# Optimization experiments

Hardware: AMD Instinct MI355X
Metric: run time of the kernel (lower is better)

The kernel has to match this reference:

```python
import jax, jax.numpy as jnp
import numpy as np

VOCAB = 50000
EMB = 200        # embedding_size
CAP = 3          # capitalization_size
IN = EMB + CAP   # LSTM input size = 203
HID = 128        # LSTMCell(128)
B = 256
T = 500          # comment_length
NC = 6           # num_classes
DENSE = 64


def _lstm_scan(x_tbi, W, b):
    """x_tbi: [T,B,IN]. W: [IN+HID, 4*HID] (tf gate order i, j, f, o), b: [4*HID].
    Returns h sequence [T,B,HID]. forget_bias=1.0 as in tf.contrib.rnn.LSTMCell."""
    h0 = jnp.zeros((x_tbi.shape[1], HID), x_tbi.dtype)

    def step(carry, x):
        h, c = carry
        gates = jnp.concatenate([x, h], axis=-1) @ W + b   # [B, 4*HID]
        i, j, f, o = jnp.split(gates, 4, axis=-1)
        c = jax.nn.sigmoid(f + 1.0) * c + jax.nn.sigmoid(i) * jnp.tanh(j)
        h = jax.nn.sigmoid(o) * jnp.tanh(c)
        return (h, c), h

    _, hs = jax.lax.scan(step, (h0, h0), x_tbi)
    return hs


def setup_inputs() -> dict:
    key = jax.random.key(0)
    ks = jax.random.split(key, 12)
    words = jax.random.randint(ks[0], (B, T), 0, VOCAB, dtype=jnp.int32)
    capitals = jax.random.randint(ks[1], (B, T), 0, CAP, dtype=jnp.int32)
    # word embeddings: random trainable table with a trailing zero-padding row
    word_emb = jax.random.normal(ks[2], (VOCAB + 1, EMB), dtype=jnp.float32) * 0.1
    # capitalization embedding: one_hot_embedding_matrix(3) = [eye(3); zeros(1,3)]
    cap_emb = jnp.concatenate([jnp.eye(CAP, dtype=jnp.float32),
                               jnp.zeros((1, CAP), dtype=jnp.float32)], axis=0)
    def glorot(k, shape):
        lim = np.sqrt(6.0 / (shape[0] + shape[1]))
        return jax.random.uniform(k, shape, jnp.float32, -lim, lim)
    W_fw = glorot(ks[3], (IN + HID, 4 * HID))
    b_fw = jnp.zeros((4 * HID,), jnp.float32)
    W_bw = glorot(ks[4], (IN + HID, 4 * HID))
    b_bw = jnp.zeros((4 * HID,), jnp.float32)
    W1 = glorot(ks[5], (2 * HID, DENSE))
    b1 = jnp.zeros((DENSE,), jnp.float32)
    W2 = glorot(ks[6], (DENSE, NC))
    b2 = jnp.zeros((NC,), jnp.float32)
    return {"words": words, "capitals": capitals, "word_emb": word_emb,
            "cap_emb": cap_emb, "W_fw": W_fw, "b_fw": b_fw,
            "W_bw": W_bw, "b_bw": b_bw, "W1": W1, "b1": b1,
            "W2": W2, "b2": b2}


def reference(words, capitals, word_emb, cap_emb, W_fw, b_fw, W_bw, b_bw,
              W1, b1, W2, b2):
    # embedding lookups and concat -> [B, T, 203]
    x = jnp.concatenate([word_emb[words], cap_emb[capitals]], axis=-1)
    x_tbi = jnp.transpose(x, (1, 0, 2))                    # [T, B, IN]
    # forward direction: take output at last timestep
    h_fw_last = _lstm_scan(x_tbi, W_fw, b_fw)[-1]          # [B, HID]
    # backward direction: bidirectional_dynamic_rnn reverses bw outputs back,
    # so outputs[1][:, 0, :] == last state of scan over the reversed sequence
    h_bw_first = _lstm_scan(x_tbi[::-1], W_bw, b_bw)[-1]   # [B, HID]
    rnn_output = jnp.concatenate([h_fw_last, h_bw_first], axis=1)  # [B, 256]
    dense1 = jax.nn.elu(rnn_output @ W1 + b1)              # [B, 64]
    y_hat = jax.nn.sigmoid(dense1 @ W2 + b2)               # [B, NC]
    return y_hat
```

## Files before the change

### kernel.cpp

```cpp
#include <hip/hip_runtime.h>

#define T 500
#define NB 256
#define VROWS 50001
#define EMB 200
#define KPAD 224
#define LOG2E 1.44269504f

typedef unsigned short u16;
typedef __attribute__((ext_vector_type(8))) __bf16 bf16x8;
typedef __attribute__((ext_vector_type(8))) short short8;
typedef __attribute__((ext_vector_type(8))) u16 u16x8;
typedef __attribute__((ext_vector_type(4))) float f32x4;
typedef __attribute__((ext_vector_type(4))) u16 u16x4;

#define AS1 __attribute__((address_space(1)))
#define AS3 __attribute__((address_space(3)))

__device__ __forceinline__ u16 f2bf(float x) {
  __bf16 h = (__bf16)x;
  return __builtin_bit_cast(u16, h);
}
__device__ __forceinline__ float bf2f(u16 b) {
  union { unsigned u; float f; } v; v.u = ((unsigned)b) << 16;
  return v.f;
}
__device__ __forceinline__ float rcp_(float x) { return __builtin_amdgcn_rcpf(x); }
__device__ __forceinline__ float ex2_(float x) { return __builtin_amdgcn_exp2f(x); }
__device__ __forceinline__ float gsc(int g) { return (g == 1) ? 2.f * LOG2E : -LOG2E; }

__global__ void prep_kernel(const float* __restrict__ cap_emb,
                            const float* __restrict__ Wfw, const float* __restrict__ bfw,
                            const float* __restrict__ Wbw, const float* __restrict__ bbw,
                            float* __restrict__ Cproj, u16* __restrict__ Bt) {
  const int S2 = 2 * 512 * KPAD;
  const int S3 = 2 * 4 * 512;
  int tid = blockIdx.x * blockDim.x + threadIdx.x;
  int nthr = gridDim.x * blockDim.x;
  for (int i = tid; i < S2 + S3; i += nthr) {
    if (i < S2) {
      int d = i / (512 * KPAD), rem = i - d * (512 * KPAD);
      int colp = rem / KPAD, k = rem - colp * KPAD;
      const float* W = d ? Wbw : Wfw;
      int g = colp & 3, jj = colp >> 2;
      Bt[i] = (k < EMB) ? f2bf(W[k * 512 + g * 128 + jj] * gsc(g)) : (u16)0;
    } else {
      int idx = i - S2;
      int dir = idx >> 11; int c = (idx >> 9) & 3; int colp = idx & 511;
      int j = colp >> 2, g = colp & 3;
      const float* W = dir ? Wbw : Wfw;
      const float* bias = dir ? bbw : bfw;
      float v = bias[g * 128 + j] + (g == 2 ? 1.f : 0.f);
      #pragma unroll
      for (int cc = 0; cc < 3; ++cc)
        v += cap_emb[c * 3 + cc] * W[(200 + cc) * 512 + g * 128 + j];
      Cproj[idx] = v * gsc(g);
    }
  }
}

__global__ __launch_bounds__(256) void xproj_kernel(
    const int* __restrict__ words, const int* __restrict__ caps,
    const float* __restrict__ word_emb, const u16* __restrict__ Bt,
    const float* __restrict__ Cproj, u16* __restrict__ XP) {
  const int bid = blockIdx.x;
  const int xcd = bid & 7, slot = bid >> 3;
  const int mt = (slot >> 3) * 8 + xcd;
  const int inner = slot & 7;
  const int nt = inner & 3, dir = inner >> 2;

  const u16* __restrict__ B = Bt + (size_t)dir * 512 * KPAD;
  u16* __restrict__ xp = XP + (size_t)dir * T * NB * 512;

  __shared__ __align__(16) char pool[34048];
  u16* As = (u16*)pool;
  u16* Bs = (u16*)(pool + 16384);
  float (*Cls)[132] = (float(*)[132])pool;

  const int tid = threadIdx.x;
  const int w = tid >> 6, l = tid & 63;
  const int la = l & 15, lb = l >> 4;
  const int wr = w >> 1, wc = w & 1;
  const int tblk = mt >> 1;
  const int bbase = (mt & 1) * 128;
  const int n0 = nt * 128;

  const int arow = tid >> 1, khalf = tid & 1;
  const int wd = words[(bbase + arow) * T + tblk];
  const float* __restrict__ aemb = word_emb + (size_t)wd * EMB;
  const int aswz0 = (arow * 4 + ((khalf * 2 + 0) ^ (arow & 3))) * 8;
  const int aswz1 = (arow * 4 + ((khalf * 2 + 1) ^ (arow & 3))) * 8;

  const int s0 = w * 128 + l, s1 = w * 128 + 64 + l;
  const int brn0 = s0 >> 2, bc0 = (s0 & 3) ^ (brn0 & 3);
  const int brn1 = s1 >> 2, bc1 = (s1 & 3) ^ (brn1 & 3);
  const u16* bsrc0 = B + (size_t)(n0 + brn0) * KPAD + bc0 * 8;
  const u16* bsrc1 = B + (size_t)(n0 + brn1) * KPAD + bc1 * 8;

  f32x4 va[4];
  auto loadA = [&](int ks) {
    #pragma unroll
    for (int q = 0; q < 4; ++q)
      va[q] = *(const f32x4*)(aemb + ks * 32 + khalf * 16 + q * 4);
  };
  auto writeA = [&](int buf) {
    u16x8 lo, hi;
    #pragma unroll
    for (int e = 0; e < 4; ++e) {
      lo[e] = f2bf(va[0][e]); lo[4 + e] = f2bf(va[1][e]);
      hi[e] = f2bf(va[2][e]); hi[4 + e] = f2bf(va[3][e]);
    }
    *(u16x8*)&As[buf * 4096 + aswz0] = lo;
    *(u16x8*)&As[buf * 4096 + aswz1] = hi;
  };
  auto stageB = [&](int buf, int ks) {
    __builtin_amdgcn_global_load_lds(
        (const AS1 void*)(bsrc0 + ks * 32),
        (AS3 void*)&Bs[buf * 4096 + (w * 128) * 8], 16, 0, 0);
    __builtin_amdgcn_global_load_lds(
        (const AS1 void*)(bsrc1 + ks * 32),
        (AS3 void*)&Bs[buf * 4096 + (w * 128 + 64) * 8], 16, 0, 0);
  };

  f32x4 z = {0.f, 0.f, 0.f, 0.f};
  f32x4 acc[4][4] = {{z,z,z,z},{z,z,z,z},{z,z,z,z},{z,z,z,z}};

  loadA(0);
  stageB(0, 0);
  writeA(0);
  __syncthreads();

  #pragma unroll 1
  for (int ks = 0; ks < 7; ++ks) {
    const int cur = ks & 1;
    if (ks < 6) { stageB(cur ^ 1, ks + 1); loadA(ks + 1); }
    bf16x8 af[4], bfr[4];
    #pragma unroll
    for (int m = 0; m < 4; ++m) {
      int ra = wr * 64 + m * 16 + la;
      af[m] = *(const bf16x8*)&As[cur * 4096 + ra * 32 + ((lb ^ (ra & 3)) * 8)];
    }
    #pragma unroll
    for (int n = 0; n < 4; ++n) {
      int rn = wc * 64 + n * 16 + la;
      bfr[n] = *(const bf16x8*)&Bs[cur * 4096 + rn * 32 + ((lb ^ (rn & 3)) * 8)];
    }
    #pragma unroll
    for (int m = 0; m < 4; ++m)
      #pragma unroll
      for (int n = 0; n < 4; ++n)
        acc[m][n] = __builtin_amdgcn_mfma_f32_16x16x32_bf16(af[m], bfr[n], acc[m][n], 0, 0, 0);
    if (ks < 6) writeA(cur ^ 1);
    __syncthreads();
  }

  const int rrow = tid >> 1, rch = tid & 1;
  const int rb = bbase + rrow;
  const int rcap = caps[rb * T + tblk];
  const float* __restrict__ cbase = Cproj + (dir * 4 + rcap) * 512;
  u16* __restrict__ rop = xp + ((size_t)tblk * NB + rb) * 512;

  #pragma unroll
  for (int pass = 0; pass < 2; ++pass) {
    if (wc == pass) {
      #pragma unroll
      for (int m = 0; m < 4; ++m)
        #pragma unroll
        for (int n = 0; n < 4; ++n)
          *(f32x4*)&Cls[n * 16 + la][wr * 64 + m * 16 + lb * 4] = acc[m][n];
    }
    __syncthreads();
    int colp0 = n0 + pass * 64 + rch * 32;
    #pragma unroll
    for (int s = 0; s < 4; ++s) {
      u16x8 o;
      #pragma unroll
      for (int e = 0; e < 8; ++e) {
        int cl = rch * 32 + s * 8 + e;
        o[e] = f2bf(Cls[cl][rrow] + cbase[colp0 + s * 8 + e]);
      }
      *(u16x8*)(rop + colp0 + s * 8) = o;
    }
    __syncthreads();
  }
}

template <int PAR>
__device__ __forceinline__ void lstm_step(
    int t, int dir, int la, int lb, int j,
    const u16* __restrict__ xpd, int voff0, int voff1, int voff2, int voff3,
    const bf16x8 (&bfrag)[4][4], u16* __restrict__ hbuf,
    u16x4 (&xc)[4],
    u16x4 (&xg)[4],
    f32x4& cst, f32x4& hl) {
  const u16* hb = hbuf + PAR * 2048;
  const int swz = (la & 7) << 3;
  bf16x8 afr[4];
  #pragma unroll
  for (int kk = 0; kk < 4; ++kk)
    afr[kk] = *(const bf16x8*)(hb + ((la * 128 + kk * 32 + lb * 8) ^ swz));

  {
    int ts = t + 2; if (ts > T - 1) ts = T - 1;
    int tt = dir ? (T - 1 - ts) : ts;
    const u16* p = xpd + (size_t)tt * (NB * 512);
    xg[0] = *(const u16x4*)(p + voff0);
    xg[1] = *(const u16x4*)(p + voff1);
    xg[2] = *(const u16x4*)(p + voff2);
    xg[3] = *(const u16x4*)(p + voff3);
  }

  f32x4 acc0, acc1, acc2, acc3;
  #pragma unroll
  for (int r = 0; r < 4; ++r) {
    acc0[r] = bf2f(xc[r][0]);
    acc1[r] = bf2f(xc[r][1]);
    acc2[r] = bf2f(xc[r][2]);
    acc3[r] = bf2f(xc[r][3]);
  }
  __builtin_amdgcn_s_setprio(1);
  #pragma unroll
  for (int kk = 0; kk < 4; ++kk) {
    acc0 = __builtin_amdgcn_mfma_f32_16x16x32_bf16(afr[kk], bfrag[0][kk], acc0, 0, 0, 0);
    acc1 = __builtin_amdgcn_mfma_f32_16x16x32_bf16(afr[kk], bfrag[1][kk], acc1, 0, 0, 0);
    acc2 = __builtin_amdgcn_mfma_f32_16x16x32_bf16(afr[kk], bfrag[2][kk], acc2, 0, 0, 0);
    acc3 = __builtin_amdgcn_mfma_f32_16x16x32_bf16(afr[kk], bfrag[3][kk], acc3, 0, 0, 0);
  }
  __builtin_amdgcn_s_setprio(0);
  u16* ho = hbuf + (PAR ^ 1) * 2048;
  #pragma unroll
  for (int r = 0; r < 4; ++r) {
    float ei = ex2_(acc0[r]);
    float ej = ex2_(acc1[r]);
    float ef = ex2_(acc2[r]);
    float eo = ex2_(acc3[r]);
    float pij = (1.f + ei) * (1.f + ej);
    float pf  = 1.f + ef;
    float num = cst[r] * pij + (ej - 1.f) * pf;
    float cn  = num * rcp_(pij * pf);
    cst[r] = cn;
    float E = ex2_(2.f * LOG2E * cn);
    float hn = (E - 1.f) * rcp_((1.f + eo) * (1.f + E));
    hl[r] = hn;
    int row = lb * 4 + r;
    ho[(row * 128 + j) ^ ((row & 7) << 3)] = f2bf(hn);
  }
  __builtin_amdgcn_sched_barrier(0);
  asm volatile("s_waitcnt lgkmcnt(0)");
  __builtin_amdgcn_s_barrier();
  __builtin_amdgcn_sched_barrier(0);
}

__global__ __launch_bounds__(512, 1) void lstm_kernel(
    const u16* __restrict__ XP, const float* __restrict__ Wfw,
    const float* __restrict__ Wbw, float* __restrict__ rnn) {
  const int dir = blockIdx.x & 1;
  const int chunk = blockIdx.x >> 1;
  const int b0 = chunk * 16;
  const u16* __restrict__ xpd = XP + (size_t)dir * T * NB * 512;
  const float* __restrict__ W = dir ? Wbw : Wfw;

  const int tid = threadIdx.x;
  const int w = tid >> 6, l = tid & 63, la = l & 15, lb = l >> 4;
  const int j = w * 16 + la;

  const int voff0 = (b0 + lb * 4 + 0) * 512 + j * 4;
  const int voff1 = (b0 + lb * 4 + 1) * 512 + j * 4;
  const int voff2 = (b0 + lb * 4 + 2) * 512 + j * 4;
  const int voff3 = (b0 + lb * 4 + 3) * 512 + j * 4;

  bf16x8 bfrag[4][4];
  #pragma unroll
  for (int g = 0; g < 4; ++g) {
    #pragma unroll
    for (int kk = 0; kk < 4; ++kk) {
      short8 t8;
      #pragma unroll
      for (int r = 0; r < 8; ++r) {
        int k = kk * 32 + lb * 8 + r;
        t8[r] = (short)f2bf(W[(203 + k) * 512 + g * 128 + j] * gsc(g));
      }
      bfrag[g][kk] = __builtin_bit_cast(bf16x8, t8);
    }
  }

  __shared__ u16 hbuf[2 * 16 * 128];
  for (int i = tid; i < 2 * 16 * 128; i += 512) hbuf[i] = 0;

  f32x4 cst = {0.f, 0.f, 0.f, 0.f};
  f32x4 hl  = {0.f, 0.f, 0.f, 0.f};

  u16x4 xA[4], xB[4], xC[4], xD[4];
  {
    int tt0 = dir ? (T - 1) : 0;
    int tt1 = dir ? (T - 2) : 1;
    const u16* p0 = xpd + (size_t)tt0 * (NB * 512);
    const u16* p1 = xpd + (size_t)tt1 * (NB * 512);
    xA[0] = *(const u16x4*)(p0 + voff0); xA[1] = *(const u16x4*)(p0 + voff1);
    xA[2] = *(const u16x4*)(p0 + voff2); xA[3] = *(const u16x4*)(p0 + voff3);
    xB[0] = *(const u16x4*)(p1 + voff0); xB[1] = *(const u16x4*)(p1 + voff1);
    xB[2] = *(const u16x4*)(p1 + voff2); xB[3] = *(const u16x4*)(p1 + voff3);
  }
  __syncthreads();

  #pragma unroll 1
  for (int tq = 0; tq < T / 4; ++tq) {
    int t0 = 4 * tq;
    lstm_step<0>(t0,     dir, la, lb, j, xpd, voff0, voff1, voff2, voff3,
                 bfrag, hbuf, xA, xC, cst, hl);
    lstm_step<1>(t0 + 1, dir, la, lb, j, xpd, voff0, voff1, voff2, voff3,
                 bfrag, hbuf, xB, xD, cst, hl);
    lstm_step<0>(t0 + 2, dir, la, lb, j, xpd, voff0, voff1, voff2, voff3,
                 bfrag, hbuf, xC, xA, cst, hl);
    lstm_step<1>(t0 + 3, dir, la, lb, j, xpd, voff0, voff1, voff2, voff3,
                 bfrag, hbuf, xD, xB, cst, hl);
  }

  #pragma unroll
  for (int r = 0; r < 4; ++r)
    rnn[(size_t)(b0 + lb * 4 + r) * 256 + dir * 128 + j] = hl[r];
}

__global__ void head_kernel(const float* __restrict__ rnn, const float* __restrict__ W1,
                            const float* __restrict__ b1, const float* __restrict__ W2,
                            const float* __restrict__ b2, float* __restrict__ out) {
  int b = blockIdx.x;
  int jj = threadIdx.x;
  __shared__ float d1[64];
  float acc = b1[jj];
  const float* r = rnn + b * 256;
  #pragma unroll 4
  for (int k = 0; k < 256; ++k) acc += r[k] * W1[k * 64 + jj];
  d1[jj] = acc > 0.f ? acc : (__expf(acc) - 1.f);
  __syncthreads();
  if (jj < 6) {
    float a2 = b2[jj];
    #pragma unroll 8
    for (int k = 0; k < 64; ++k) a2 += d1[k] * W2[k * 6 + jj];
    out[b * 6 + jj] = rcp_(1.f + __expf(-a2));
  }
}

extern "C" void kernel_launch(void* const* d_in, const int* in_sizes, int n_in,
                              void* d_out, int out_size, void* d_ws, size_t ws_size,
                              hipStream_t stream) {
  (void)in_sizes; (void)n_in; (void)out_size; (void)ws_size;
  const int*   words    = (const int*)  d_in[0];
  const int*   caps     = (const int*)  d_in[1];
  const float* word_emb = (const float*)d_in[2];
  const float* cap_emb  = (const float*)d_in[3];
  const float* Wfw      = (const float*)d_in[4];
  const float* bfw      = (const float*)d_in[5];
  const float* Wbw      = (const float*)d_in[6];
  const float* bbw      = (const float*)d_in[7];
  const float* W1       = (const float*)d_in[8];
  const float* b1       = (const float*)d_in[9];
  const float* W2       = (const float*)d_in[10];
  const float* b2       = (const float*)d_in[11];
  float* out = (float*)d_out;

  char* base = (char*)d_ws;
  size_t off = 0;
  auto alloc = [&](size_t bytes) {
    char* q = base + off;
    off = (off + bytes + 255) & ~(size_t)255;
    return q;
  };
  u16*   XP     = (u16*)  alloc((size_t)2 * T * NB * 512 * 2);
  u16*   Bt     = (u16*)  alloc((size_t)2 * 512 * KPAD * 2);
  float* Cproj  = (float*)alloc((size_t)2 * 4 * 512 * 4);
  float* rnn    = (float*)alloc((size_t)256 * 256 * 4);

  hipLaunchKernelGGL(prep_kernel, dim3(256), dim3(256), 0, stream,
                     cap_emb, Wfw, bfw, Wbw, bbw, Cproj, Bt);
  hipLaunchKernelGGL(xproj_kernel, dim3(8000), dim3(256), 0, stream,
                     words, caps, word_emb, Bt, Cproj, XP);
  hipLaunchKernelGGL(lstm_kernel, dim3(32), dim3(512), 0, stream,
                     XP, Wfw, Wbw, rnn);
  hipLaunchKernelGGL(head_kernel, dim3(256), dim3(64), 0, stream,
                     rnn, W1, b1, W2, b2, out);
}
```

Baseline: 627.3 us.

## Stage embedding rows once per block and loop over all output tiles; transpose LSTM MFMA

The input-projection kernel now gathers the 128 embedding rows for a timestep block into shared memory once. It then loops over all eight direction/column tiles, instead of launching a separate block per tile that re-gathers the same rows. This removes redundant gather and bf16-conversion traffic, at the cost of fewer, larger 512-thread blocks and a big A buffer in LDS. The LSTM step swaps the MFMA operand order so each lane owns contiguous gate values for one batch row. That gives vectorized 16-byte XP loads, packed h stores to LDS and a vector store of the final state.

```diff
diff --git a/kernel.cpp b/kernel.cpp
--- a/kernel.cpp
+++ b/kernel.cpp
@@ -59,139 +59,126 @@
   }
 }
 
-__global__ __launch_bounds__(256) void xproj_kernel(
+__global__ __launch_bounds__(512) void xproj_kernel(
     const int* __restrict__ words, const int* __restrict__ caps,
     const float* __restrict__ word_emb, const u16* __restrict__ Bt,
     const float* __restrict__ Cproj, u16* __restrict__ XP) {
-  const int bid = blockIdx.x;
-  const int xcd = bid & 7, slot = bid >> 3;
-  const int mt = (slot >> 3) * 8 + xcd;
-  const int inner = slot & 7;
-  const int nt = inner & 3, dir = inner >> 2;
-
-  const u16* __restrict__ B = Bt + (size_t)dir * 512 * KPAD;
-  u16* __restrict__ xp = XP + (size_t)dir * T * NB * 512;
-
+  const int mt = blockIdx.x;
+  const int tblk = mt >> 1;
+  const int bbase = (mt & 1) * 128;
+
+  __shared__ __align__(16) u16 As[128 * 256];
   __shared__ __align__(16) char pool[34048];
-  u16* As = (u16*)pool;
-  u16* Bs = (u16*)(pool + 16384);
+  u16* Bs = (u16*)pool;
   float (*Cls)[132] = (float(*)[132])pool;
 
   const int tid = threadIdx.x;
   const int w = tid >> 6, l = tid & 63;
   const int la = l & 15, lb = l >> 4;
   const int wr = w >> 1, wc = w & 1;
-  const int tblk = mt >> 1;
-  const int bbase = (mt & 1) * 128;
-  const int n0 = nt * 128;
-
-  const int arow = tid >> 1, khalf = tid & 1;
-  const int wd = words[(bbase + arow) * T + tblk];
-  const float* __restrict__ aemb = word_emb + (size_t)wd * EMB;
-  const int aswz0 = (arow * 4 + ((khalf * 2 + 0) ^ (arow & 3))) * 8;
-  const int aswz1 = (arow * 4 + ((khalf * 2 + 1) ^ (arow & 3))) * 8;
-
-  const int s0 = w * 128 + l, s1 = w * 128 + 64 + l;
-  const int brn0 = s0 >> 2, bc0 = (s0 & 3) ^ (brn0 & 3);
-  const int brn1 = s1 >> 2, bc1 = (s1 & 3) ^ (brn1 & 3);
-  const u16* bsrc0 = B + (size_t)(n0 + brn0) * KPAD + bc0 * 8;
-  const u16* bsrc1 = B + (size_t)(n0 + brn1) * KPAD + bc1 * 8;
-
-  f32x4 va[4];
-  auto loadA = [&](int ks) {
-    #pragma unroll
-    for (int q = 0; q < 4; ++q)
-      va[q] = *(const f32x4*)(aemb + ks * 32 + khalf * 16 + q * 4);
-  };
-  auto writeA = [&](int buf) {
-    u16x8 lo, hi;
-    #pragma unroll
-    for (int e = 0; e < 4; ++e) {
-      lo[e] = f2bf(va[0][e]); lo[4 + e] = f2bf(va[1][e]);
-      hi[e] = f2bf(va[2][e]); hi[4 + e] = f2bf(va[3][e]);
-    }
-    *(u16x8*)&As[buf * 4096 + aswz0] = lo;
-    *(u16x8*)&As[buf * 4096 + aswz1] = hi;
-  };
-  auto stageB = [&](int buf, int ks) {
-    __builtin_amdgcn_global_load_lds(
-        (const AS1 void*)(bsrc0 + ks * 32),
-        (AS3 void*)&Bs[buf * 4096 + (w * 128) * 8], 16, 0, 0);
-    __builtin_amdgcn_global_load_lds(
-        (const AS1 void*)(bsrc1 + ks * 32),
-        (AS3 void*)&Bs[buf * 4096 + (w * 128 + 64) * 8], 16, 0, 0);
-  };
-
-  f32x4 z = {0.f, 0.f, 0.f, 0.f};
-  f32x4 acc[4][4] = {{z,z,z,z},{z,z,z,z},{z,z,z,z},{z,z,z,z}};
-
-  loadA(0);
-  stageB(0, 0);
-  writeA(0);
+
+  for (int i = tid; i < 128 * 28; i += 512) {
+    int r = i / 28, c = i - r * 28;
+    u16x8 o;
+    if (c < 25) {
+      int wd = words[(bbase + r) * T + tblk];
+      const float* p = word_emb + (size_t)wd * EMB + c * 8;
+      f32x4 v0 = *(const f32x4*)p;
+      f32x4 v1 = *(const f32x4*)(p + 4);
+      #pragma unroll
+      for (int e = 0; e < 4; ++e) { o[e] = f2bf(v0[e]); o[4 + e] = f2bf(v1[e]); }
+    } else {
+      o = u16x8{0,0,0,0,0,0,0,0};
+    }
+    *(u16x8*)&As[r * 256 + ((c ^ (r & 7)) * 8)] = o;
+  }
   __syncthreads();
 
-  #pragma unroll 1
-  for (int ks = 0; ks < 7; ++ks) {
-    const int cur = ks & 1;
-    if (ks < 6) { stageB(cur ^ 1, ks + 1); loadA(ks + 1); }
-    bf16x8 af[4], bfr[4];
-    #pragma unroll
-    for (int m = 0; m < 4; ++m) {
-      int ra = wr * 64 + m * 16 + la;
-      af[m] = *(const bf16x8*)&As[cur * 4096 + ra * 32 + ((lb ^ (ra & 3)) * 8)];
-    }
-    #pragma unroll
-    for (int n = 0; n < 4; ++n) {
-      int rn = wc * 64 + n * 16 + la;
-      bfr[n] = *(const bf16x8*)&Bs[cur * 4096 + rn * 32 + ((lb ^ (rn & 3)) * 8)];
-    }
-    #pragma unroll
-    for (int m = 0; m < 4; ++m)
-      #pragma unroll
-      for (int n = 0; n < 4; ++n)
-        acc[m][n] = __builtin_amdgcn_mfma_f32_16x16x32_bf16(af[m], bfr[n], acc[m][n], 0, 0, 0);
-    if (ks < 6) writeA(cur ^ 1);
-    __syncthreads();
-  }
-
-  const int rrow = tid >> 1, rch = tid & 1;
+  const int s_ = w * 64 + l;
+  const int brn = s_ >> 2, bd = s_ & 3;
+  const int bc = bd ^ (brn & 3);
+
+  const int rrow = tid >> 2, rch = tid & 3;
   const int rb = bbase + rrow;
   const int rcap = caps[rb * T + tblk];
-  const float* __restrict__ cbase = Cproj + (dir * 4 + rcap) * 512;
-  u16* __restrict__ rop = xp + ((size_t)tblk * NB + rb) * 512;
-
-  #pragma unroll
-  for (int pass = 0; pass < 2; ++pass) {
-    if (wc == pass) {
-      #pragma unroll
-      for (int m = 0; m < 4; ++m)
+
+  #pragma unroll 1
+  for (int combo = 0; combo < 8; ++combo) {
+    const int dir = combo >> 2, nt = combo & 3;
+    const u16* __restrict__ B = Bt + (size_t)dir * 512 * KPAD;
+    u16* __restrict__ xp = XP + (size_t)dir * T * NB * 512;
+    const int n0 = nt * 128;
+    const u16* bsrc = B + (size_t)(n0 + brn) * KPAD + bc * 8;
+
+    auto stageB = [&](int buf, int ks) {
+      __builtin_amdgcn_global_load_lds(
+          (const AS1 void*)(bsrc + ks * 32),
+          (AS3 void*)&Bs[buf * 4096 + w * 512], 16, 0, 0);
+    };
+
+    f32x4 z = {0.f, 0.f, 0.f, 0.f};
+    f32x4 acc[2][4] = {{z,z,z,z},{z,z,z,z}};
+
+    stageB(0, 0);
+    __syncthreads();
+    #pragma unroll 1
+    for (int ks = 0; ks < 7; ++ks) {
+      const int cur = ks & 1;
+      if (ks < 6) stageB(cur ^ 1, ks + 1);
+      bf16x8 af[2], bfr[4];
+      #pragma unroll
+      for (int m = 0; m < 2; ++m) {
+        int ra = wr * 32 + m * 16 + la;
+        af[m] = *(const bf16x8*)&As[ra * 256 + (((ks * 4 + lb) ^ (ra & 7)) * 8)];
+      }
+      #pragma unroll
+      for (int n = 0; n < 4; ++n) {
+        int rn = wc * 64 + n * 16 + la;
+        bfr[n] = *(const bf16x8*)&Bs[cur * 4096 + rn * 32 + ((lb ^ (rn & 3)) * 8)];
+      }
+      #pragma unroll
+      for (int m = 0; m < 2; ++m)
         #pragma unroll
         for (int n = 0; n < 4; ++n)
-          *(f32x4*)&Cls[n * 16 + la][wr * 64 + m * 16 + lb * 4] = acc[m][n];
-    }
-    __syncthreads();
-    int colp0 = n0 + pass * 64 + rch * 32;
+          acc[m][n] = __builtin_amdgcn_mfma_f32_16x16x32_bf16(af[m], bfr[n], acc[m][n], 0, 0, 0);
+      __syncthreads();
+    }
+
+    const float* __restrict__ cbase = Cproj + (dir * 4 + rcap) * 512;
+    u16* __restrict__ rop = xp + ((size_t)tblk * NB + rb) * 512;
     #pragma unroll
-    for (int s = 0; s < 4; ++s) {
-      u16x8 o;
-      #pragma unroll
-      for (int e = 0; e < 8; ++e) {
-        int cl = rch * 32 + s * 8 + e;
-        o[e] = f2bf(Cls[cl][rrow] + cbase[colp0 + s * 8 + e]);
-      }
-      *(u16x8*)(rop + colp0 + s * 8) = o;
-    }
-    __syncthreads();
+    for (int pass = 0; pass < 2; ++pass) {
+      if (wc == pass) {
+        #pragma unroll
+        for (int m = 0; m < 2; ++m)
+          #pragma unroll
+          for (int n = 0; n < 4; ++n)
+            *(f32x4*)&Cls[n * 16 + la][wr * 32 + m * 16 + lb * 4] = acc[m][n];
+      }
+      __syncthreads();
+      int colp0 = n0 + pass * 64 + rch * 16;
+      #pragma unroll
+      for (int s = 0; s < 2; ++s) {
+        u16x8 o;
+        #pragma unroll
+        for (int e = 0; e < 8; ++e) {
+          int cl = rch * 16 + s * 8 + e;
+          o[e] = f2bf(Cls[cl][rrow] + cbase[colp0 + s * 8 + e]);
+        }
+        *(u16x8*)(rop + colp0 + s * 8) = o;
+      }
+      __syncthreads();
+    }
   }
 }
 
 template <int PAR>
 __device__ __forceinline__ void lstm_step(
-    int t, int dir, int la, int lb, int j,
-    const u16* __restrict__ xpd, int voff0, int voff1, int voff2, int voff3,
+    int t, int dir, int la, int lb, int w,
+    const u16* __restrict__ xpd, int voff,
     const bf16x8 (&bfrag)[4][4], u16* __restrict__ hbuf,
-    u16x4 (&xc)[4],
-    u16x4 (&xg)[4],
+    u16x8 (&xc)[2],
+    u16x8 (&xg)[2],
     f32x4& cst, f32x4& hl) {
   const u16* hb = hbuf + PAR * 2048;
   const int swz = (la & 7) << 3;
@@ -203,31 +190,32 @@
   {
     int ts = t + 2; if (ts > T - 1) ts = T - 1;
     int tt = dir ? (T - 1 - ts) : ts;
-    const u16* p = xpd + (size_t)tt * (NB * 512);
-    xg[0] = *(const u16x4*)(p + voff0);
-    xg[1] = *(const u16x4*)(p + voff1);
-    xg[2] = *(const u16x4*)(p + voff2);
-    xg[3] = *(const u16x4*)(p + voff3);
+    const u16* p = xpd + (size_t)tt * (NB * 512) + voff;
+    xg[0] = *(const u16x8*)p;
+    xg[1] = *(const u16x8*)(p + 8);
   }
 
   f32x4 acc0, acc1, acc2, acc3;
   #pragma unroll
   for (int r = 0; r < 4; ++r) {
-    acc0[r] = bf2f(xc[r][0]);
-    acc1[r] = bf2f(xc[r][1]);
-    acc2[r] = bf2f(xc[r][2]);
-    acc3[r] = bf2f(xc[r][3]);
+    const u16x8& xh = (r < 2) ? xc[0] : xc[1];
+    int base = (r & 1) * 4;
+    acc0[r] = bf2f(xh[base + 0]);
+    acc1[r] = bf2f(xh[base + 1]);
+    acc2[r] = bf2f(xh[base + 2]);
+    acc3[r] = bf2f(xh[base + 3]);
   }
   __builtin_amdgcn_s_setprio(1);
   #pragma unroll
   for (int kk = 0; kk < 4; ++kk) {
-    acc0 = __builtin_amdgcn_mfma_f32_16x16x32_bf16(afr[kk], bfrag[0][kk], acc0, 0, 0, 0);
-    acc1 = __builtin_amdgcn_mfma_f32_16x16x32_bf16(afr[kk], bfrag[1][kk], acc1, 0, 0, 0);
-    acc2 = __builtin_amdgcn_mfma_f32_16x16x32_bf16(afr[kk], bfrag[2][kk], acc2, 0, 0, 0);
-    acc3 = __builtin_amdgcn_mfma_f32_16x16x32_bf16(afr[kk], bfrag[3][kk], acc3, 0, 0, 0);
+    acc0 = __builtin_amdgcn_mfma_f32_16x16x32_bf16(bfrag[0][kk], afr[kk], acc0, 0, 0, 0);
+    acc1 = __builtin_amdgcn_mfma_f32_16x16x32_bf16(bfrag[1][kk], afr[kk], acc1, 0, 0, 0);
+    acc2 = __builtin_amdgcn_mfma_f32_16x16x32_bf16(bfrag[2][kk], afr[kk], acc2, 0, 0, 0);
+    acc3 = __builtin_amdgcn_mfma_f32_16x16x32_bf16(bfrag[3][kk], afr[kk], acc3, 0, 0, 0);
   }
   __builtin_amdgcn_s_setprio(0);
   u16* ho = hbuf + (PAR ^ 1) * 2048;
+  u16x4 hw;
   #pragma unroll
   for (int r = 0; r < 4; ++r) {
     float ei = ex2_(acc0[r]);
@@ -242,9 +230,9 @@
     float E = ex2_(2.f * LOG2E * cn);
     float hn = (E - 1.f) * rcp_((1.f + eo) * (1.f + E));
     hl[r] = hn;
-    int row = lb * 4 + r;
-    ho[(row * 128 + j) ^ ((row & 7) << 3)] = f2bf(hn);
-  }
+    hw[r] = f2bf(hn);
+  }
+  *(u16x4*)&ho[(la * 128 + w * 16 + lb * 4) ^ swz] = hw;
   __builtin_amdgcn_sched_barrier(0);
   asm volatile("s_waitcnt lgkmcnt(0)");
   __builtin_amdgcn_s_barrier();
@@ -264,10 +252,7 @@
   const int w = tid >> 6, l = tid & 63, la = l & 15, lb = l >> 4;
   const int j = w * 16 + la;
 
-  const int voff0 = (b0 + lb * 4 + 0) * 512 + j * 4;
-  const int voff1 = (b0 + lb * 4 + 1) * 512 + j * 4;
-  const int voff2 = (b0 + lb * 4 + 2) * 512 + j * 4;
-  const int voff3 = (b0 + lb * 4 + 3) * 512 + j * 4;
+  const int voff = (b0 + la) * 512 + w * 64 + lb * 16;
 
   bf16x8 bfrag[4][4];
   #pragma unroll
@@ -290,35 +275,27 @@
   f32x4 cst = {0.f, 0.f, 0.f, 0.f};
   f32x4 hl  = {0.f, 0.f, 0.f, 0.f};
 
-  u16x4 xA[4], xB[4], xC[4], xD[4];
+  u16x8 xA[2], xB[2], xC[2], xD[2];
   {
     int tt0 = dir ? (T - 1) : 0;
     int tt1 = dir ? (T - 2) : 1;
-    const u16* p0 = xpd + (size_t)tt0 * (NB * 512);
-    const u16* p1 = xpd + (size_t)tt1 * (NB * 512);
-    xA[0] = *(const u16x4*)(p0 + voff0); xA[1] = *(const u16x4*)(p0 + voff1);
-    xA[2] = *(const u16x4*)(p0 + voff2); xA[3] = *(const u16x4*)(p0 + voff3);
-    xB[0] = *(const u16x4*)(p1 + voff0); xB[1] = *(const u16x4*)(p1 + voff1);
-    xB[2] = *(const u16x4*)(p1 + voff2); xB[3] = *(const u16x4*)(p1 + voff3);
+    const u16* p0 = xpd + (size_t)tt0 * (NB * 512) + voff;
+    const u16* p1 = xpd + (size_t)tt1 * (NB * 512) + voff;
+    xA[0] = *(const u16x8*)p0; xA[1] = *(const u16x8*)(p0 + 8);
+    xB[0] = *(const u16x8*)p1; xB[1] = *(const u16x8*)(p1 + 8);
   }
   __syncthreads();
 
   #pragma unroll 1
   for (int tq = 0; tq < T / 4; ++tq) {
     int t0 = 4 * tq;
-    lstm_step<0>(t0,     dir, la, lb, j, xpd, voff0, voff1, voff2, voff3,
-                 bfrag, hbuf, xA, xC, cst, hl);
-    lstm_step<1>(t0 + 1, dir, la, lb, j, xpd, voff0, voff1, voff2, voff3,
-                 bfrag, hbuf, xB, xD, cst, hl);
-    lstm_step<0>(t0 + 2, dir, la, lb, j, xpd, voff0, voff1, voff2, voff3,
-                 bfrag, hbuf, xC, xA, cst, hl);
-    lstm_step<1>(t0 + 3, dir, la, lb, j, xpd, voff0, voff1, voff2, voff3,
-                 bfrag, hbuf, xD, xB, cst, hl);
-  }
-
-  #pragma unroll
-  for (int r = 0; r < 4; ++r)
-    rnn[(size_t)(b0 + lb * 4 + r) * 256 + dir * 128 + j] = hl[r];
+    lstm_step<0>(t0,     dir, la, lb, w, xpd, voff, bfrag, hbuf, xA, xC, cst, hl);
+    lstm_step<1>(t0 + 1, dir, la, lb, w, xpd, voff, bfrag, hbuf, xB, xD, cst, hl);
+    lstm_step<0>(t0 + 2, dir, la, lb, w, xpd, voff, bfrag, hbuf, xC, xA, cst, hl);
+    lstm_step<1>(t0 + 3, dir, la, lb, w, xpd, voff, bfrag, hbuf, xD, xB, cst, hl);
+  }
+
+  *(f32x4*)&rnn[(size_t)(b0 + la) * 256 + dir * 128 + w * 16 + lb * 4] = hl;
 }
 
 __global__ void head_kernel(const float* __restrict__ rnn, const float* __restrict__ W1,
@@ -373,7 +350,7 @@
 
   hipLaunchKernelGGL(prep_kernel, dim3(256), dim3(256), 0, stream,
                      cap_emb, Wfw, bfw, Wbw, bbw, Cproj, Bt);
-  hipLaunchKernelGGL(xproj_kernel, dim3(8000), dim3(256), 0, stream,
+  hipLaunchKernelGGL(xproj_kernel, dim3(1000), dim3(512), 0, stream,
                      words, caps, word_emb, Bt, Cproj, XP);
   hipLaunchKernelGGL(lstm_kernel, dim3(32), dim3(512), 0, stream,
                      XP, Wfw, Wbw, rnn);
```

After: 652.5 us. 4.0% more time.
